# Kernel optimization log

Hardware: AMD Instinct MI355X
Metric: run time of the kernel (lower is better)

## Reference

```python
import jax, jax.numpy as jnp
import numpy as np

N, E = 50000, 1_000_000
IN_F, OUT_F = 128, 64
NEG_SLOPE = 0.2


def setup_inputs() -> dict:
    key = jax.random.key(0)
    k1, k2, k3, k4, k5 = jax.random.split(key, 5)
    x = jax.random.normal(k1, (N, IN_F), dtype=jnp.float32)
    edge_index = jax.random.randint(k2, (2, E), 0, N, dtype=jnp.int64)
    # xavier_uniform with gain=1.414 (as in the torch init)
    gain = 1.414
    bW = gain * np.sqrt(6.0 / (IN_F + OUT_F))
    W = jax.random.uniform(k3, (IN_F, OUT_F), jnp.float32, -bW, bW)
    ba = gain * np.sqrt(6.0 / (OUT_F + 1))
    a_src = jax.random.uniform(k4, (OUT_F, 1), jnp.float32, -ba, ba)
    a_dst = jax.random.uniform(k5, (OUT_F, 1), jnp.float32, -ba, ba)
    return {"x": x, "edge_index": edge_index, "W": W, "a_src": a_src, "a_dst": a_dst}


def reference(x, edge_index, W, a_src, a_dst):
    n = x.shape[0]
    Wh = x @ W                                  # [N, F_out]
    src = edge_index[0]
    dst = edge_index[1]
    # per-edge attention logits: (Wh[src] . a_src) + (Wh[dst] . a_dst)
    s_src = Wh @ a_src[:, 0]                    # [N]
    s_dst = Wh @ a_dst[:, 0]                    # [N]
    e = jax.nn.leaky_relu(s_src[src] + s_dst[dst], negative_slope=NEG_SLOPE)  # [E]
    e = jnp.exp(e - jnp.max(e))                 # global-max stabilized exp (matches torch code)
    denom = jax.ops.segment_sum(e, dst, num_segments=n) + 1e-16  # [N]
    alpha = e / denom[dst]                      # [E]  (dropout p=0 -> identity)
    out = jax.ops.segment_sum(Wh[src] * alpha[:, None], dst, num_segments=n)  # [N, F_out]
    return jax.nn.elu(out)
```

## Files before the change

kernel.cpp:

```cpp
#include <hip/hip_runtime.h>
#include <hip/hip_bf16.h>
#include <math.h>

#define NN 50000
#define NE 1000000
#define FIN 128
#define FOUT 64
#define NEG 0.2f

#define NB   2048
#define DPB  25
#define NBUSED 2000
#define TS   4096
#define NT   245

using short8  = __attribute__((ext_vector_type(8))) short;
using floatx4 = __attribute__((ext_vector_type(4))) float;

static __device__ __forceinline__ short f2bf(float f) {
    __hip_bfloat16 h = __float2bfloat16(f);
    return *(short*)&h;
}

__global__ __launch_bounds__(256) void k_gemm(
    const float* __restrict__ x, const float* __restrict__ W,
    const float* __restrict__ a_src, const float* __restrict__ a_dst,
    __hip_bfloat16* __restrict__ Whb, float* __restrict__ s_src,
    float* __restrict__ s_dst)
{
    const int lane = threadIdx.x & 63;
    const int wave = threadIdx.x >> 6;
    const int col  = lane & 15;
    const int quad = lane >> 4;

    const int strip = blockIdx.x * 4 + wave;
    if (strip >= NN / 16) return;
    const int row0 = strip * 16;

    short8 bfr[4][4];
    #pragma unroll
    for (int kk = 0; kk < 4; ++kk) {
        #pragma unroll
        for (int nt = 0; nt < 4; ++nt) {
            const float* wp = W + (kk * 32 + quad * 8) * FOUT + nt * 16 + col;
            #pragma unroll
            for (int j = 0; j < 8; ++j)
                bfr[kk][nt][j] = f2bf(wp[j * FOUT]);
        }
    }

    floatx4 acc[4] = {{0.f,0.f,0.f,0.f},{0.f,0.f,0.f,0.f},
                      {0.f,0.f,0.f,0.f},{0.f,0.f,0.f,0.f}};

    const float* xrow = x + (size_t)(row0 + col) * FIN + quad * 8;
    #pragma unroll
    for (int kk = 0; kk < 4; ++kk) {
        const float4 u0 = *(const float4*)(xrow + kk * 32);
        const float4 u1 = *(const float4*)(xrow + kk * 32 + 4);
        short8 af;
        af[0] = f2bf(u0.x); af[1] = f2bf(u0.y);
        af[2] = f2bf(u0.z); af[3] = f2bf(u0.w);
        af[4] = f2bf(u1.x); af[5] = f2bf(u1.y);
        af[6] = f2bf(u1.z); af[7] = f2bf(u1.w);
        #pragma unroll
        for (int nt = 0; nt < 4; ++nt)
            acc[nt] = __builtin_amdgcn_mfma_f32_16x16x32_bf16(
                af, bfr[kk][nt], acc[nt], 0, 0, 0);
    }

    const float av0 = a_src[col], av1 = a_src[16 + col];
    const float av2 = a_src[32 + col], av3 = a_src[48 + col];
    const float bv0 = a_dst[col], bv1 = a_dst[16 + col];
    const float bv2 = a_dst[32 + col], bv3 = a_dst[48 + col];

    float ps[4], pd[4];
    #pragma unroll
    for (int reg = 0; reg < 4; ++reg) {
        ps[reg] = acc[0][reg] * av0 + acc[1][reg] * av1
                + acc[2][reg] * av2 + acc[3][reg] * av3;
        pd[reg] = acc[0][reg] * bv0 + acc[1][reg] * bv1
                + acc[2][reg] * bv2 + acc[3][reg] * bv3;
    }

    #pragma unroll
    for (int nt = 0; nt < 4; ++nt)
        #pragma unroll
        for (int reg = 0; reg < 4; ++reg)
            Whb[(size_t)(row0 + quad * 4 + reg) * FOUT + nt * 16 + col] =
                __float2bfloat16(acc[nt][reg]);

    #pragma unroll
    for (int off = 1; off < 16; off <<= 1) {
        #pragma unroll
        for (int reg = 0; reg < 4; ++reg) {
            ps[reg] += __shfl_xor(ps[reg], off);
            pd[reg] += __shfl_xor(pd[reg], off);
        }
    }
    if (col == 0) {
        #pragma unroll
        for (int reg = 0; reg < 4; ++reg) {
            s_src[row0 + quad * 4 + reg] = ps[reg];
            s_dst[row0 + quad * 4 + reg] = pd[reg];
        }
    }
}

__global__ __launch_bounds__(512) void k_tilesort(
    const int* __restrict__ ei, unsigned* __restrict__ bdata,
    int* __restrict__ gofs)
{
    __shared__ int cnt[NB];
    __shared__ int cur[NB];
    __shared__ unsigned srt[TS];
    __shared__ int wsum[8];

    const int tile = blockIdx.x;
    const int tid = threadIdx.x;
    const int base = tile * TS;
    const int tcnt = (NE - base < TS) ? (NE - base) : TS;

    for (int i = tid; i < NB; i += 512) cnt[i] = 0;
    __syncthreads();

    unsigned pk[8];
    #pragma unroll
    for (int j = 0; j < 8; ++j) {
        const int i = j * 512 + tid;
        if (i < tcnt) {
            const int e = base + i;
            const unsigned s = (unsigned)__builtin_nontemporal_load(ei + e);
            const unsigned d = (unsigned)__builtin_nontemporal_load(ei + NE + e);
            pk[j] = (s << 16) | d;
            atomicAdd(&cnt[d / DPB], 1);
        } else pk[j] = 0xFFFFFFFFu;
    }
    __syncthreads();

    {
        const int lane = tid & 63, wv = tid >> 6;
        const int i0 = tid * 4;
        const int v0 = cnt[i0], v1 = cnt[i0 + 1];
        const int v2 = cnt[i0 + 2], v3 = cnt[i0 + 3];
        const int s = v0 + v1 + v2 + v3;
        int inc = s;
        #pragma unroll
        for (int off = 1; off < 64; off <<= 1) {
            const int t = __shfl_up(inc, off);
            if (lane >= off) inc += t;
        }
        if (lane == 63) wsum[wv] = inc;
        __syncthreads();
        int wb = 0;
        #pragma unroll
        for (int w = 0; w < 7; ++w) if (w < wv) wb += wsum[w];
        const int excl = wb + inc - s;
        cur[i0]     = excl;
        cur[i0 + 1] = excl + v0;
        cur[i0 + 2] = excl + v0 + v1;
        cur[i0 + 3] = excl + v0 + v1 + v2;
        int4 g = make_int4(excl, excl + v0, excl + v0 + v1, excl + v0 + v1 + v2);
        *(int4*)(gofs + (size_t)tile * NB + i0) = g;
    }
    __syncthreads();

    #pragma unroll
    for (int j = 0; j < 8; ++j) {
        if (pk[j] != 0xFFFFFFFFu) {
            const int b = (int)(pk[j] & 0xffffu) / DPB;
            const int pos = atomicAdd(&cur[b], 1);
            srt[pos] = pk[j];
        }
    }
    __syncthreads();

    for (int i = tid; i < tcnt; i += 512)
        bdata[base + i] = srt[i];
}

__global__ __launch_bounds__(256) void k_sortgather(
    const int* __restrict__ gofs, const unsigned* __restrict__ bdata,
    const float* __restrict__ s_src, const float* __restrict__ s_dst,
    const __hip_bfloat16* __restrict__ Whb, float* __restrict__ out)
{
    __shared__ unsigned raw[1024];
    __shared__ unsigned srt[1024];
    __shared__ int cnt[32];
    __shared__ int ofs2[33];
    __shared__ int cur[32];
    __shared__ int wsum[4];

    const int b = blockIdx.x;
    const int tid = threadIdx.x;
    const int lane = tid & 63;
    const int wv = tid >> 6;
    const int d0 = b * DPB;

    if (tid < 32) cnt[tid] = 0;

    int c = 0, o = 0;
    if (tid < NT) {
        o = gofs[tid * NB + b];
        const int tc = (tid < NT - 1) ? TS : (NE - (NT - 1) * TS);
        const int nxt = (b < NB - 1) ? gofs[tid * NB + b + 1] : tc;
        c = nxt - o;
    }
    int inc = c;
    #pragma unroll
    for (int off = 1; off < 64; off <<= 1) {
        const int t = __shfl_up(inc, off);
        if (lane >= off) inc += t;
    }
    if (lane == 63) wsum[wv] = inc;
    __syncthreads();
    int wb = 0;
    #pragma unroll
    for (int w = 0; w < 3; ++w) if (w < wv) wb += wsum[w];
    const int segbase = wb + inc - c;
    const int tot = wsum[0] + wsum[1] + wsum[2] + wsum[3];

    for (int k = 0; k < c; ++k)
        raw[segbase + k] = bdata[(size_t)tid * TS + o + k];
    __syncthreads();

    for (int i = tid; i < tot; i += 256)
        atomicAdd(&cnt[(int)(raw[i] & 0xffffu) - d0], 1);
    __syncthreads();

    if (tid < 32) {
        const int cc = (tid < DPB) ? cnt[tid] : 0;
        int in2 = cc;
        #pragma unroll
        for (int off = 1; off < 32; off <<= 1) {
            const int t = __shfl_up(in2, off);
            if (tid >= off) in2 += t;
        }
        ofs2[tid + 1] = in2;
        if (tid == 0) ofs2[0] = 0;
        cur[tid] = in2 - cc;
    }
    __syncthreads();

    for (int i = tid; i < tot; i += 256) {
        const unsigned p = raw[i];
        const int j = (int)(p & 0xffffu) - d0;
        const int pos = atomicAdd(&cur[j], 1);
        srt[pos] = p;
    }
    __syncthreads();

    for (int j = wv; j < DPB; j += 4) {
        const int d = d0 + j;
        const float sd = s_dst[d];
        const int beg = ofs2[j];
        const int end = ofs2[j + 1];
        float acc = 0.f, den = 0.f;
        int i = beg;
        for (; i + 4 <= end; i += 4) {
            const unsigned p0 = srt[i];
            const unsigned p1 = srt[i + 1];
            const unsigned p2 = srt[i + 2];
            const unsigned p3 = srt[i + 3];
            const int s0 = p0 >> 16, s1 = p1 >> 16, s2 = p2 >> 16, s3 = p3 >> 16;
            float v0 = s_src[s0] + sd; v0 = (v0 > 0.f) ? v0 : NEG * v0;
            float v1 = s_src[s1] + sd; v1 = (v1 > 0.f) ? v1 : NEG * v1;
            float v2 = s_src[s2] + sd; v2 = (v2 > 0.f) ? v2 : NEG * v2;
            float v3 = s_src[s3] + sd; v3 = (v3 > 0.f) ? v3 : NEG * v3;
            const float e0 = __expf(v0);
            const float e1 = __expf(v1);
            const float e2 = __expf(v2);
            const float e3 = __expf(v3);
            acc = fmaf(e0, __bfloat162float(Whb[(size_t)s0 * FOUT + lane]), acc);
            acc = fmaf(e1, __bfloat162float(Whb[(size_t)s1 * FOUT + lane]), acc);
            acc = fmaf(e2, __bfloat162float(Whb[(size_t)s2 * FOUT + lane]), acc);
            acc = fmaf(e3, __bfloat162float(Whb[(size_t)s3 * FOUT + lane]), acc);
            den += (e0 + e1) + (e2 + e3);
        }
        for (; i < end; ++i) {
            const unsigned p0 = srt[i];
            const int s0 = p0 >> 16;
            float v0 = s_src[s0] + sd; v0 = (v0 > 0.f) ? v0 : NEG * v0;
            const float e0 = __expf(v0);
            acc = fmaf(e0, __bfloat162float(Whb[(size_t)s0 * FOUT + lane]), acc);
            den += e0;
        }
        const float r = acc / (den + 1e-16f);
        out[(size_t)d * FOUT + lane] = (r > 0.f) ? r : expm1f(r);
    }
}

extern "C" void kernel_launch(void* const* d_in, const int* in_sizes, int n_in,
                              void* d_out, int out_size, void* d_ws, size_t ws_size,
                              hipStream_t stream)
{
    const float* x     = (const float*)d_in[0];
    const int*   ei    = (const int*)d_in[1];
    const float* W     = (const float*)d_in[2];
    const float* a_src = (const float*)d_in[3];
    const float* a_dst = (const float*)d_in[4];
    float* out = (float*)d_out;

    float* ws    = (float*)d_ws;
    __hip_bfloat16* Whb = (__hip_bfloat16*)ws;
    float* s_src = ws + (size_t)NN * FOUT / 2;
    float* s_dst = s_src + NN;
    int*   gofs  = (int*)(s_dst + NN);
    unsigned* bdata = (unsigned*)(gofs + (size_t)NT * NB);

    k_gemm<<<(NN / 16 + 3) / 4, 256, 0, stream>>>(x, W, a_src, a_dst,
                                                  Whb, s_src, s_dst);
    k_tilesort<<<NT, 512, 0, stream>>>(ei, bdata, gofs);
    k_sortgather<<<NBUSED, 256, 0, stream>>>(gofs, bdata, s_src, s_dst, Whb, out);
}
```

Baseline: 138.8 us.

## Merge GEMM and tile sort into one launch, transpose offsets, precompute edge exps

```diff
diff --git a/kernel.cpp b/kernel.cpp
--- a/kernel.cpp
+++ b/kernel.cpp
@@ -13,6 +13,8 @@
 #define NBUSED 2000
 #define TS   4096
 #define NT   245
+#define NTP  256
+#define GEMM_BLKS 782
 
 using short8  = __attribute__((ext_vector_type(8))) short;
 using floatx4 = __attribute__((ext_vector_type(4))) float;
@@ -22,111 +24,111 @@
     return *(short*)&h;
 }
 
-__global__ __launch_bounds__(256) void k_gemm(
+__global__ __launch_bounds__(256) void k_front(
     const float* __restrict__ x, const float* __restrict__ W,
     const float* __restrict__ a_src, const float* __restrict__ a_dst,
+    const int* __restrict__ ei,
     __hip_bfloat16* __restrict__ Whb, float* __restrict__ s_src,
-    float* __restrict__ s_dst)
-{
-    const int lane = threadIdx.x & 63;
-    const int wave = threadIdx.x >> 6;
-    const int col  = lane & 15;
-    const int quad = lane >> 4;
-
-    const int strip = blockIdx.x * 4 + wave;
-    if (strip >= NN / 16) return;
-    const int row0 = strip * 16;
-
-    short8 bfr[4][4];
-    #pragma unroll
-    for (int kk = 0; kk < 4; ++kk) {
-        #pragma unroll
-        for (int nt = 0; nt < 4; ++nt) {
-            const float* wp = W + (kk * 32 + quad * 8) * FOUT + nt * 16 + col;
-            #pragma unroll
-            for (int j = 0; j < 8; ++j)
-                bfr[kk][nt][j] = f2bf(wp[j * FOUT]);
-        }
-    }
-
-    floatx4 acc[4] = {{0.f,0.f,0.f,0.f},{0.f,0.f,0.f,0.f},
-                      {0.f,0.f,0.f,0.f},{0.f,0.f,0.f,0.f}};
-
-    const float* xrow = x + (size_t)(row0 + col) * FIN + quad * 8;
-    #pragma unroll
-    for (int kk = 0; kk < 4; ++kk) {
-        const float4 u0 = *(const float4*)(xrow + kk * 32);
-        const float4 u1 = *(const float4*)(xrow + kk * 32 + 4);
-        short8 af;
-        af[0] = f2bf(u0.x); af[1] = f2bf(u0.y);
-        af[2] = f2bf(u0.z); af[3] = f2bf(u0.w);
-        af[4] = f2bf(u1.x); af[5] = f2bf(u1.y);
-        af[6] = f2bf(u1.z); af[7] = f2bf(u1.w);
-        #pragma unroll
-        for (int nt = 0; nt < 4; ++nt)
-            acc[nt] = __builtin_amdgcn_mfma_f32_16x16x32_bf16(
-                af, bfr[kk][nt], acc[nt], 0, 0, 0);
-    }
-
-    const float av0 = a_src[col], av1 = a_src[16 + col];
-    const float av2 = a_src[32 + col], av3 = a_src[48 + col];
-    const float bv0 = a_dst[col], bv1 = a_dst[16 + col];
-    const float bv2 = a_dst[32 + col], bv3 = a_dst[48 + col];
-
-    float ps[4], pd[4];
-    #pragma unroll
-    for (int reg = 0; reg < 4; ++reg) {
-        ps[reg] = acc[0][reg] * av0 + acc[1][reg] * av1
-                + acc[2][reg] * av2 + acc[3][reg] * av3;
-        pd[reg] = acc[0][reg] * bv0 + acc[1][reg] * bv1
-                + acc[2][reg] * bv2 + acc[3][reg] * bv3;
-    }
-
-    #pragma unroll
-    for (int nt = 0; nt < 4; ++nt)
-        #pragma unroll
-        for (int reg = 0; reg < 4; ++reg)
-            Whb[(size_t)(row0 + quad * 4 + reg) * FOUT + nt * 16 + col] =
-                __float2bfloat16(acc[nt][reg]);
-
-    #pragma unroll
-    for (int off = 1; off < 16; off <<= 1) {
-        #pragma unroll
-        for (int reg = 0; reg < 4; ++reg) {
-            ps[reg] += __shfl_xor(ps[reg], off);
-            pd[reg] += __shfl_xor(pd[reg], off);
-        }
-    }
-    if (col == 0) {
-        #pragma unroll
-        for (int reg = 0; reg < 4; ++reg) {
-            s_src[row0 + quad * 4 + reg] = ps[reg];
-            s_dst[row0 + quad * 4 + reg] = pd[reg];
-        }
-    }
-}
-
-__global__ __launch_bounds__(512) void k_tilesort(
-    const int* __restrict__ ei, unsigned* __restrict__ bdata,
-    int* __restrict__ gofs)
+    float* __restrict__ s_dst,
+    unsigned* __restrict__ bdata, int* __restrict__ gofs)
 {
     __shared__ int cnt[NB];
     __shared__ int cur[NB];
     __shared__ unsigned srt[TS];
-    __shared__ int wsum[8];
-
-    const int tile = blockIdx.x;
-    const int tid = threadIdx.x;
+    __shared__ int wsum[4];
+
+    const int tid  = threadIdx.x;
+    const int lane = tid & 63;
+    const int wv   = tid >> 6;
+
+    if (blockIdx.x < GEMM_BLKS) {
+        const int col  = lane & 15;
+        const int quad = lane >> 4;
+        const int strip = blockIdx.x * 4 + wv;
+        if (strip >= NN / 16) return;
+        const int row0 = strip * 16;
+
+        short8 bfr[4][4];
+        #pragma unroll
+        for (int kk = 0; kk < 4; ++kk) {
+            #pragma unroll
+            for (int nt = 0; nt < 4; ++nt) {
+                const float* wp = W + (kk * 32 + quad * 8) * FOUT + nt * 16 + col;
+                #pragma unroll
+                for (int j = 0; j < 8; ++j)
+                    bfr[kk][nt][j] = f2bf(wp[j * FOUT]);
+            }
+        }
+
+        floatx4 acc[4] = {{0.f,0.f,0.f,0.f},{0.f,0.f,0.f,0.f},
+                          {0.f,0.f,0.f,0.f},{0.f,0.f,0.f,0.f}};
+
+        const float* xrow = x + (size_t)(row0 + col) * FIN + quad * 8;
+        #pragma unroll
+        for (int kk = 0; kk < 4; ++kk) {
+            const float4 u0 = *(const float4*)(xrow + kk * 32);
+            const float4 u1 = *(const float4*)(xrow + kk * 32 + 4);
+            short8 af;
+            af[0] = f2bf(u0.x); af[1] = f2bf(u0.y);
+            af[2] = f2bf(u0.z); af[3] = f2bf(u0.w);
+            af[4] = f2bf(u1.x); af[5] = f2bf(u1.y);
+            af[6] = f2bf(u1.z); af[7] = f2bf(u1.w);
+            #pragma unroll
+            for (int nt = 0; nt < 4; ++nt)
+                acc[nt] = __builtin_amdgcn_mfma_f32_16x16x32_bf16(
+                    af, bfr[kk][nt], acc[nt], 0, 0, 0);
+        }
+
+        const float av0 = a_src[col], av1 = a_src[16 + col];
+        const float av2 = a_src[32 + col], av3 = a_src[48 + col];
+        const float bv0 = a_dst[col], bv1 = a_dst[16 + col];
+        const float bv2 = a_dst[32 + col], bv3 = a_dst[48 + col];
+
+        float ps[4], pd[4];
+        #pragma unroll
+        for (int reg = 0; reg < 4; ++reg) {
+            ps[reg] = acc[0][reg] * av0 + acc[1][reg] * av1
+                    + acc[2][reg] * av2 + acc[3][reg] * av3;
+            pd[reg] = acc[0][reg] * bv0 + acc[1][reg] * bv1
+                    + acc[2][reg] * bv2 + acc[3][reg] * bv3;
+        }
+
+        #pragma unroll
+        for (int nt = 0; nt < 4; ++nt)
+            #pragma unroll
+            for (int reg = 0; reg < 4; ++reg)
+                Whb[(size_t)(row0 + quad * 4 + reg) * FOUT + nt * 16 + col] =
+                    __float2bfloat16(acc[nt][reg]);
+
+        #pragma unroll
+        for (int off = 1; off < 16; off <<= 1) {
+            #pragma unroll
+            for (int reg = 0; reg < 4; ++reg) {
+                ps[reg] += __shfl_xor(ps[reg], off);
+                pd[reg] += __shfl_xor(pd[reg], off);
+            }
+        }
+        if (col == 0) {
+            #pragma unroll
+            for (int reg = 0; reg < 4; ++reg) {
+                s_src[row0 + quad * 4 + reg] = ps[reg];
+                s_dst[row0 + quad * 4 + reg] = pd[reg];
+            }
+        }
+        return;
+    }
+
+    const int tile = blockIdx.x - GEMM_BLKS;
     const int base = tile * TS;
     const int tcnt = (NE - base < TS) ? (NE - base) : TS;
 
-    for (int i = tid; i < NB; i += 512) cnt[i] = 0;
-    __syncthreads();
-
-    unsigned pk[8];
+    for (int i = tid; i < NB; i += 256) cnt[i] = 0;
+    __syncthreads();
+
+    unsigned pk[16];
     #pragma unroll
-    for (int j = 0; j < 8; ++j) {
-        const int i = j * 512 + tid;
+    for (int j = 0; j < 16; ++j) {
+        const int i = j * 256 + tid;
         if (i < tcnt) {
             const int e = base + i;
             const unsigned s = (unsigned)__builtin_nontemporal_load(ei + e);
@@ -138,11 +140,10 @@
     __syncthreads();
 
     {
-        const int lane = tid & 63, wv = tid >> 6;
-        const int i0 = tid * 4;
-        const int v0 = cnt[i0], v1 = cnt[i0 + 1];
-        const int v2 = cnt[i0 + 2], v3 = cnt[i0 + 3];
-        const int s = v0 + v1 + v2 + v3;
+        const int i0 = tid * 8;
+        int v[8], s = 0;
+        #pragma unroll
+        for (int j = 0; j < 8; ++j) { v[j] = cnt[i0 + j]; s += v[j]; }
         int inc = s;
         #pragma unroll
         for (int off = 1; off < 64; off <<= 1) {
@@ -153,19 +154,18 @@
         __syncthreads();
         int wb = 0;
         #pragma unroll
-        for (int w = 0; w < 7; ++w) if (w < wv) wb += wsum[w];
-        const int excl = wb + inc - s;
-        cur[i0]     = excl;
-        cur[i0 + 1] = excl + v0;
-        cur[i0 + 2] = excl + v0 + v1;
-        cur[i0 + 3] = excl + v0 + v1 + v2;
-        int4 g = make_int4(excl, excl + v0, excl + v0 + v1, excl + v0 + v1 + v2);
-        *(int4*)(gofs + (size_t)tile * NB + i0) = g;
+        for (int w = 0; w < 3; ++w) if (w < wv) wb += wsum[w];
+        int excl = wb + inc - s;
+        int g[8];
+        #pragma unroll
+        for (int j = 0; j < 8; ++j) { cur[i0 + j] = excl; g[j] = excl; excl += v[j]; }
+        *(int4*)(gofs + (size_t)tile * NB + i0)     = make_int4(g[0], g[1], g[2], g[3]);
+        *(int4*)(gofs + (size_t)tile * NB + i0 + 4) = make_int4(g[4], g[5], g[6], g[7]);
     }
     __syncthreads();
 
     #pragma unroll
-    for (int j = 0; j < 8; ++j) {
+    for (int j = 0; j < 16; ++j) {
         if (pk[j] != 0xFFFFFFFFu) {
             const int b = (int)(pk[j] & 0xffffu) / DPB;
             const int pos = atomicAdd(&cur[b], 1);
@@ -174,17 +174,37 @@
     }
     __syncthreads();
 
-    for (int i = tid; i < tcnt; i += 512)
+    for (int i = tid; i < tcnt; i += 256)
         bdata[base + i] = srt[i];
 }
 
+__global__ __launch_bounds__(256) void k_transp(
+    const int* __restrict__ gofs, int* __restrict__ gofs_t)
+{
+    __shared__ int tb[32][33];
+    const int bi = blockIdx.x & 63;
+    const int ti = blockIdx.x >> 6;
+    const int r = threadIdx.x >> 5;
+    const int c = threadIdx.x & 31;
+    for (int rr = r; rr < 32; rr += 8) {
+        const int t = ti * 32 + rr;
+        tb[rr][c] = (t < NT) ? gofs[(size_t)t * NB + bi * 32 + c] : 0;
+    }
+    __syncthreads();
+    for (int rr = r; rr < 32; rr += 8) {
+        const int b = bi * 32 + rr;
+        gofs_t[(size_t)b * NTP + ti * 32 + c] = tb[c][rr];
+    }
+}
+
 __global__ __launch_bounds__(256) void k_sortgather(
-    const int* __restrict__ gofs, const unsigned* __restrict__ bdata,
+    const int* __restrict__ gofs_t, const unsigned* __restrict__ bdata,
     const float* __restrict__ s_src, const float* __restrict__ s_dst,
     const __hip_bfloat16* __restrict__ Whb, float* __restrict__ out)
 {
     __shared__ unsigned raw[1024];
     __shared__ unsigned srt[1024];
+    __shared__ float evs[1024];
     __shared__ int cnt[32];
     __shared__ int ofs2[33];
     __shared__ int cur[32];
@@ -200,10 +220,8 @@
 
     int c = 0, o = 0;
     if (tid < NT) {
-        o = gofs[tid * NB + b];
-        const int tc = (tid < NT - 1) ? TS : (NE - (NT - 1) * TS);
-        const int nxt = (b < NB - 1) ? gofs[tid * NB + b + 1] : tc;
-        c = nxt - o;
+        o = gofs_t[(size_t)b * NTP + tid];
+        c = gofs_t[(size_t)(b + 1) * NTP + tid] - o;
     }
     int inc = c;
     #pragma unroll
@@ -249,38 +267,39 @@
     }
     __syncthreads();
 
+    for (int i = tid; i < tot; i += 256) {
+        const unsigned p = srt[i];
+        float v = s_src[p >> 16] + s_dst[p & 0xffffu];
+        v = (v > 0.f) ? v : NEG * v;
+        evs[i] = __expf(v);
+    }
+    __syncthreads();
+
     for (int j = wv; j < DPB; j += 4) {
         const int d = d0 + j;
-        const float sd = s_dst[d];
         const int beg = ofs2[j];
         const int end = ofs2[j + 1];
         float acc = 0.f, den = 0.f;
         int i = beg;
-        for (; i + 4 <= end; i += 4) {
-            const unsigned p0 = srt[i];
-            const unsigned p1 = srt[i + 1];
-            const unsigned p2 = srt[i + 2];
-            const unsigned p3 = srt[i + 3];
-            const int s0 = p0 >> 16, s1 = p1 >> 16, s2 = p2 >> 16, s3 = p3 >> 16;
-            float v0 = s_src[s0] + sd; v0 = (v0 > 0.f) ? v0 : NEG * v0;
-            float v1 = s_src[s1] + sd; v1 = (v1 > 0.f) ? v1 : NEG * v1;
-            float v2 = s_src[s2] + sd; v2 = (v2 > 0.f) ? v2 : NEG * v2;
-            float v3 = s_src[s3] + sd; v3 = (v3 > 0.f) ? v3 : NEG * v3;
-            const float e0 = __expf(v0);
-            const float e1 = __expf(v1);
-            const float e2 = __expf(v2);
-            const float e3 = __expf(v3);
-            acc = fmaf(e0, __bfloat162float(Whb[(size_t)s0 * FOUT + lane]), acc);
-            acc = fmaf(e1, __bfloat162float(Whb[(size_t)s1 * FOUT + lane]), acc);
-            acc = fmaf(e2, __bfloat162float(Whb[(size_t)s2 * FOUT + lane]), acc);
-            acc = fmaf(e3, __bfloat162float(Whb[(size_t)s3 * FOUT + lane]), acc);
-            den += (e0 + e1) + (e2 + e3);
+        for (; i + 8 <= end; i += 8) {
+            int ss[8]; float ee[8], w[8];
+            #pragma unroll
+            for (int k = 0; k < 8; ++k) {
+                ss[k] = (int)(srt[i + k] >> 16);
+                ee[k] = evs[i + k];
+            }
+            #pragma unroll
+            for (int k = 0; k < 8; ++k)
+                w[k] = __bfloat162float(Whb[(size_t)ss[k] * FOUT + lane]);
+            #pragma unroll
+            for (int k = 0; k < 8; ++k) {
+                acc = fmaf(ee[k], w[k], acc);
+                den += ee[k];
+            }
         }
         for (; i < end; ++i) {
-            const unsigned p0 = srt[i];
-            const int s0 = p0 >> 16;
-            float v0 = s_src[s0] + sd; v0 = (v0 > 0.f) ? v0 : NEG * v0;
-            const float e0 = __expf(v0);
+            const int s0 = (int)(srt[i] >> 16);
+            const float e0 = evs[i];
             acc = fmaf(e0, __bfloat162float(Whb[(size_t)s0 * FOUT + lane]), acc);
             den += e0;
         }
@@ -305,10 +324,12 @@
     float* s_src = ws + (size_t)NN * FOUT / 2;
     float* s_dst = s_src + NN;
     int*   gofs  = (int*)(s_dst + NN);
-    unsigned* bdata = (unsigned*)(gofs + (size_t)NT * NB);
-
-    k_gemm<<<(NN / 16 + 3) / 4, 256, 0, stream>>>(x, W, a_src, a_dst,
-                                                  Whb, s_src, s_dst);
-    k_tilesort<<<NT, 512, 0, stream>>>(ei, bdata, gofs);
-    k_sortgather<<<NBUSED, 256, 0, stream>>>(gofs, bdata, s_src, s_dst, Whb, out);
-}
+    int*   gofs_t = gofs + (size_t)NT * NB;
+    unsigned* bdata = (unsigned*)(gofs_t + (size_t)NB * NTP);
+
+    k_front<<<GEMM_BLKS + NT, 256, 0, stream>>>(x, W, a_src, a_dst, ei,
+                                                Whb, s_src, s_dst, bdata, gofs);
+    k_transp<<<512, 256, 0, stream>>>(gofs, gofs_t);
+    k_sortgather<<<NBUSED, 256, 0, stream>>>(gofs_t, bdata, s_src, s_dst,
+                                             Whb, out);
+}
```

Result: faster. 135.7 us (-2.2%).
